# Optimization experiments

Hardware: AMD Instinct MI355X
Metric: run time of the kernel (lower is better)

The kernel has to match this reference:

```python
import jax, jax.numpy as jnp
import numpy as np

B, N, D, C, H, W = 4, 900, 256, 256, 200, 200
HEADS, LVLS, PTS, K = 8, 1, 4, 10


def setup_inputs() -> dict:
    key = jax.random.key(0)
    ks = jax.random.split(key, 16)
    s = 0.02
    return {
        "query_embed": jax.random.normal(ks[0], (B, N, D), jnp.float32),
        "ctrl_points": jax.random.uniform(ks[1], (B, N, 4, 2), jnp.float32, -50.0, 50.0),
        "bev_features": jax.random.normal(ks[2], (B, C, H, W), jnp.float32),
        "spatial_shapes": jnp.array([[H, W]], dtype=jnp.int32),
        "pc_range": jnp.array([-51.2, -51.2, -5.0, 51.2, 51.2, 3.0], jnp.float32),
        "Wq": s * jax.random.normal(ks[3], (D, D)), "bq": jnp.zeros((D,)),
        "Wv": s * jax.random.normal(ks[4], (C, D)), "bv": jnp.zeros((D,)),
        "Woff": s * jax.random.normal(ks[5], (D, HEADS * LVLS * PTS * 2)), "boff": jnp.zeros((HEADS * LVLS * PTS * 2,)),
        "Wattn": s * jax.random.normal(ks[6], (D, HEADS * LVLS * PTS)), "battn": jnp.zeros((HEADS * LVLS * PTS,)),
        "Wmo": s * jax.random.normal(ks[7], (D, D)), "bmo": jnp.zeros((D,)),
        "Wo": s * jax.random.normal(ks[8], (D, D)), "bo": jnp.zeros((D,)),
    }


def _forward(query_embed, ctrl_points, bev_features, spatial_shapes, pc_range,
             Wq, bq, Wv, bv, Woff, boff, Wattn, battn, Wmo, bmo, Wo, bo):
    b, n, d = query_embed.shape
    _, c, h, w = bev_features.shape
    hd = d // HEADS

    # --- cubic Bezier interpolation: (B,N,4,2) -> (B,N,K,2) dense points ---
    t = jnp.linspace(0.0, 1.0, K, dtype=query_embed.dtype)
    basis = jnp.stack([(1 - t) ** 3, 3 * (1 - t) ** 2 * t, 3 * (1 - t) * t ** 2, t ** 3], axis=-1)  # (K,4)
    dense = jnp.einsum('kc,bncd->bnkd', basis, ctrl_points)
    # --- normalize to [0,1] by pc_range, clamp to [0.01,0.99] ---
    nx = (dense[..., 0] - pc_range[0]) / (pc_range[3] - pc_range[0])
    ny = (dense[..., 1] - pc_range[1]) / (pc_range[4] - pc_range[1])
    ref = jnp.clip(jnp.stack([nx, ny], axis=-1), 0.01, 0.99)  # (B,N,K,2)

    # --- projections ---
    q = query_embed @ Wq + bq                                       # (B,N,D) (identity for residual)
    v = bev_features.reshape(b, c, h * w).transpose(0, 2, 1) @ Wv + bv  # (B,HW,D)
    v = v.reshape(b, h * w, HEADS, hd)

    off = (q @ Woff + boff).reshape(b, n, HEADS, LVLS, PTS, 2)
    aw = jax.nn.softmax((q @ Wattn + battn).reshape(b, n, HEADS, LVLS * PTS), axis=-1)
    aw = aw.reshape(b, n, HEADS, PTS)  # LVLS == 1

    # offset normalizer = (W, H) per level
    normalizer = jnp.stack([spatial_shapes[..., 1], spatial_shapes[..., 0]], axis=-1).astype(q.dtype)  # (L,2)
    # sampling locations: broadcast K bezier points against heads/points offsets
    loc = ref[:, :, None, :, None, :] + off / normalizer[None, None, None, :, None, :]  # (B,N,HEADS,K,PTS,2)

    # --- bilinear sampling, align_corners=False, zero padding ---
    gx = loc[..., 0] * w - 0.5
    gy = loc[..., 1] * h - 0.5
    x0 = jnp.floor(gx)
    y0 = jnp.floor(gy)
    wx = gx - x0
    wy = gy - y0
    x0i = x0.astype(jnp.int32)
    y0i = y0.astype(jnp.int32)

    vflat = v.transpose(0, 2, 1, 3).reshape(b * HEADS, h * w, hd)  # (B*HEADS, HW, hd)

    def flat(a):  # (B,N,HEADS,K,PTS) -> (B*HEADS, N*K*PTS)
        return a.transpose(0, 2, 1, 3, 4).reshape(b * HEADS, n * K * PTS)

    acc = jnp.zeros((b * HEADS, n * K * PTS, hd), dtype=q.dtype)
    for dx, dy in ((0, 0), (1, 0), (0, 1), (1, 1)):
        ix = flat(x0i) + dx
        iy = flat(y0i) + dy
        wxx = flat(wx) if dx else (1.0 - flat(wx))
        wyy = flat(wy) if dy else (1.0 - flat(wy))
        valid = (ix >= 0) & (ix < w) & (iy >= 0) & (iy < h)
        idx = jnp.clip(iy, 0, h - 1) * w + jnp.clip(ix, 0, w - 1)
        corner = jnp.take_along_axis(vflat, idx[..., None], axis=1)  # (B*HEADS, Npts, hd)
        acc = acc + corner * (wxx * wyy * valid.astype(q.dtype))[..., None]

    sampled = acc.reshape(b, HEADS, n, K, PTS, hd)
    # weighted sum over (K, PTS); attention weights shared across the K bezier points
    out = jnp.einsum('bhnkpd,bnhp->bnhd', sampled, aw).reshape(b, n, d)
    out = out @ Wmo + bmo + q   # mmcv MSDeformAttn output_proj + residual (identity = query)
    out = out @ Wo + bo         # outer output_proj
    return out


def reference(query_embed, ctrl_points, bev_features, spatial_shapes, pc_range,
              Wq, bq, Wv, bv, Woff, boff, Wattn, battn, Wmo, bmo, Wo, bo):
    return _forward(query_embed, ctrl_points, bev_features, spatial_shapes, pc_range,
                    Wq, bq, Wv, bv, Woff, boff, Wattn, battn, Wmo, bmo, Wo, bo)
```

## Files before the change

### kernel.cpp

```cpp
#include <hip/hip_runtime.h>
#include <hip/hip_bf16.h>
#include <math.h>


typedef unsigned short u16;
typedef unsigned int u32;
typedef short bf16x8 __attribute__((ext_vector_type(8)));
typedef float f32x4 __attribute__((ext_vector_type(4)));

__device__ __forceinline__ float bf2f(u16 u) {
  union { u32 i; float f; } c; c.i = ((u32)u) << 16; return c.f;
}
__device__ __forceinline__ float bflo(u32 w) {
  union { u32 i; float f; } c; c.i = w << 16; return c.f;
}
__device__ __forceinline__ float bfhi(u32 w) {
  union { u32 i; float f; } c; c.i = w & 0xffff0000u; return c.f;
}
__device__ __forceinline__ u16 f2bf(float f) {
  union { float f; u32 i; } c; c.f = f;
  u32 u = c.i;
  return (u16)((u + 0x7FFFu + ((u >> 16) & 1u)) >> 16);
}
__device__ __forceinline__ int imin(int a, int b) { return a < b ? a : b; }
__device__ __forceinline__ int imax(int a, int b) { return a > b ? a : b; }

__device__ __forceinline__ void glds16(const u16* g, u16* l) {
  __builtin_amdgcn_global_load_lds(
      (__attribute__((address_space(1))) const void*)g,
      (__attribute__((address_space(3))) void*)l, 16, 0, 0);
}

__global__ __launch_bounds__(256) void prep_weights(
    const float* __restrict__ Wq, const float* __restrict__ Wv,
    const float* __restrict__ Woff, const float* __restrict__ Wattn,
    const float* __restrict__ Wmo, const float* __restrict__ Wo,
    const float* __restrict__ boff, const float* __restrict__ battn,
    const float* __restrict__ query,
    u16* __restrict__ wqT, u16* __restrict__ wvT, u16* __restrict__ woaT,
    u16* __restrict__ wmoT, u16* __restrict__ woT, float* __restrict__ boa,
    u16* __restrict__ qin)
{
  int idx = blockIdx.x * 256 + threadIdx.x;
  {
    int i = idx * 4;
    float4 v = *(const float4*)(query + i);
    uint2 st;
    st.x = (u32)f2bf(v.x) | ((u32)f2bf(v.y) << 16);
    st.y = (u32)f2bf(v.z) | ((u32)f2bf(v.w) << 16);
    *(uint2*)(qin + i) = st;
  }
  if (idx < 65536) {
    int r = idx >> 8, c = idx & 255;
    wqT[idx]  = f2bf(Wq[c * 256 + r]);
    wvT[idx]  = f2bf(Wv[c * 256 + r]);
    wmoT[idx] = f2bf(Wmo[c * 256 + r]);
    woT[idx]  = f2bf(Wo[c * 256 + r]);
  }
  if (idx < 96 * 256) {
    int n = idx >> 8, k = idx & 255;
    woaT[idx] = f2bf((n < 64) ? Woff[k * 64 + n] : Wattn[k * 32 + (n - 64)]);
  }
  if (idx < 96) boa[idx] = (idx < 64) ? boff[idx] : battn[idx - 64];
}

__global__ __launch_bounds__(256) void transpose_bev(
    const float* __restrict__ bev, u16* __restrict__ bevT)
{
  __shared__ u16 t[64 * 66];
  const int b = blockIdx.z, c0 = blockIdx.y * 64, p0 = blockIdx.x * 64;
  const float* src = bev + ((size_t)b * 256 + c0) * 40000 + p0;
#pragma unroll
  for (int it = 0; it < 4; ++it) {
    int slot = it * 256 + threadIdx.x;
    int r = slot >> 4, i = slot & 15;
    float4 dv = *(const float4*)(src + (size_t)r * 40000 + i * 4);
    u32* dst = (u32*)&t[r * 66 + i * 4];
    dst[0] = (u32)f2bf(dv.x) | ((u32)f2bf(dv.y) << 16);
    dst[1] = (u32)f2bf(dv.z) | ((u32)f2bf(dv.w) << 16);
  }
  __syncthreads();
  u16* ob = bevT + ((size_t)b * 40000 + p0) * 256 + c0;
#pragma unroll
  for (int it = 0; it < 2; ++it) {
    int slot = it * 256 + threadIdx.x;
    int pr = slot >> 3, ci = slot & 7;
    u32 w0 = (u32)t[(ci * 8 + 0) * 66 + pr] | ((u32)t[(ci * 8 + 1) * 66 + pr] << 16);
    u32 w1 = (u32)t[(ci * 8 + 2) * 66 + pr] | ((u32)t[(ci * 8 + 3) * 66 + pr] << 16);
    u32 w2 = (u32)t[(ci * 8 + 4) * 66 + pr] | ((u32)t[(ci * 8 + 5) * 66 + pr] << 16);
    u32 w3 = (u32)t[(ci * 8 + 6) * 66 + pr] | ((u32)t[(ci * 8 + 7) * 66 + pr] << 16);
    uint4 ov; ov.x = w0; ov.y = w1; ov.z = w2; ov.w = w3;
    *(uint4*)(ob + (size_t)pr * 256 + ci * 8) = ov;
  }
}

enum { GM_F32 = 0, GM_BF16 = 1, GM_BOTH = 2, GM_V = 3 };

template <int MODE, bool HAS_RES, bool XY_SWAP>
__global__ __launch_bounds__(256) void gemm_bt(
    const u16* __restrict__ A, const u16* __restrict__ Bt,
    const float* __restrict__ bias, const float* __restrict__ res,
    u16* __restrict__ outb, float* __restrict__ outf,
    int M, int N, int K, long long btStrideZ, long long outStrideZ)
{
  __shared__ __align__(16) u16 lA[128 * 32];
  __shared__ __align__(16) u16 lB[128 * 32];
  const int tid = threadIdx.x;
  const int wv = tid >> 6, lane = tid & 63;
  const int m0 = (XY_SWAP ? blockIdx.x : blockIdx.y) * 128;
  const int n0 = (XY_SWAP ? blockIdx.y : blockIdx.x) * 128;
  const u16* Bz = Bt + (size_t)blockIdx.z * btStrideZ;

  const int crow = lane >> 2;
  const int ckoff = (lane & 3) * 8;
  const int a1 = imin(m0 + wv * 16 + crow, M - 1);
  const int a2 = imin(m0 + (wv + 4) * 16 + crow, M - 1);
  const int b1 = imin(n0 + wv * 16 + crow, N - 1);
  const int b2 = imin(n0 + (wv + 4) * 16 + crow, N - 1);
  const u16* gA1 = A + (size_t)a1 * K + ckoff;
  const u16* gA2 = A + (size_t)a2 * K + ckoff;
  const u16* gB1 = Bz + (size_t)b1 * K + ckoff;
  const u16* gB2 = Bz + (size_t)b2 * K + ckoff;
  u16* lA1 = lA + wv * 512;  u16* lA2 = lA + (wv + 4) * 512;
  u16* lB1 = lB + wv * 512;  u16* lB2 = lB + (wv + 4) * 512;

  const int fm = (wv & 1) * 64, fn = (wv >> 1) * 64;
  const int fr = lane & 15, fk = (lane >> 4) * 8;

  f32x4 acc[4][4];
#pragma unroll
  for (int i = 0; i < 4; ++i)
#pragma unroll
    for (int j = 0; j < 4; ++j) acc[i][j] = (f32x4){0.f, 0.f, 0.f, 0.f};

  for (int k0 = 0; k0 < K; k0 += 32) {
    glds16(gA1 + k0, lA1);
    glds16(gA2 + k0, lA2);
    glds16(gB1 + k0, lB1);
    glds16(gB2 + k0, lB2);
    __syncthreads();
    bf16x8 af[4], bfv[4];
#pragma unroll
    for (int i = 0; i < 4; ++i)
      af[i] = *(const bf16x8*)&lA[(fm + i * 16 + fr) * 32 + fk];
#pragma unroll
    for (int j = 0; j < 4; ++j)
      bfv[j] = *(const bf16x8*)&lB[(fn + j * 16 + fr) * 32 + fk];
    __syncthreads();
#pragma unroll
    for (int i = 0; i < 4; ++i)
#pragma unroll
      for (int j = 0; j < 4; ++j)
        acc[i][j] = __builtin_amdgcn_mfma_f32_16x16x32_bf16(af[i], bfv[j], acc[i][j], 0, 0, 0);
  }

  const int quad = lane >> 4;
#pragma unroll
  for (int j = 0; j < 4; ++j) {
    const int n = n0 + fn + j * 16 + fr;
    const bool nok = (n < N);
    float bcol = 0.f;
    if (MODE != GM_V) bcol = bias[nok ? n : 0];
#pragma unroll
    for (int i = 0; i < 4; ++i) {
      const int mb = m0 + fm + i * 16 + quad * 4;
      if (MODE == GM_V) {
        if (nok) {
          u16 u0 = f2bf(acc[i][j][0] + bias[mb + 0]);
          u16 u1 = f2bf(acc[i][j][1] + bias[mb + 1]);
          u16 u2 = f2bf(acc[i][j][2] + bias[mb + 2]);
          u16 u3 = f2bf(acc[i][j][3] + bias[mb + 3]);
          size_t off = (size_t)blockIdx.z * outStrideZ +
                       (size_t)(mb >> 5) * (40000 * 32) + (size_t)n * 32 + (mb & 31);
          uint2 st; st.x = (u32)u0 | ((u32)u1 << 16); st.y = (u32)u2 | ((u32)u3 << 16);
          *(uint2*)(outb + off) = st;
        }
      } else {
#pragma unroll
        for (int r = 0; r < 4; ++r) {
          const int m = mb + r;
          if (m < M && nok) {
            float x = acc[i][j][r] + bcol;
            if (HAS_RES) x += res[(size_t)m * N + n];
            if (MODE == GM_F32) outf[(size_t)m * N + n] = x;
            else if (MODE == GM_BF16) outb[(size_t)m * N + n] = f2bf(x);
            else { outb[(size_t)m * N + n] = f2bf(x); outf[(size_t)m * N + n] = x; }
          }
        }
      }
    }
  }
}

__global__ __launch_bounds__(256) void sampler(
    const float* __restrict__ ctrl,
    const float* __restrict__ pc,
    const float* __restrict__ oa_,
    const u16* __restrict__ v,
    u16* __restrict__ attn_out)
{
  __shared__ int   sX0[4][40], sY0[4][40];
  __shared__ float sWx[4][40], sWy[4][40], sAw[4][40];
  const int w = threadIdx.x >> 6, lane = threadIdx.x & 63;
  const int bh = blockIdx.x & 31;
  const int n = (blockIdx.x >> 5) * 4 + w;
  const int h = bh & 7, b = bh >> 3;
  const int row = b * 900 + n;

  if (lane < 40) {
    const int k = lane >> 2, p = lane & 3;
    const float t = (float)k * (1.0f / 9.0f), u = 1.f - t;
    const float c0 = u * u * u, c1 = 3.f * u * u * t, c2 = 3.f * u * t * t, c3 = t * t * t;
    const float* cp = ctrl + (size_t)row * 8;
    float cx = c0 * cp[0] + c1 * cp[2] + c2 * cp[4] + c3 * cp[6];
    float cy = c0 * cp[1] + c1 * cp[3] + c2 * cp[5] + c3 * cp[7];
    float nx = (cx - pc[0]) / (pc[3] - pc[0]);
    float ny = (cy - pc[1]) / (pc[4] - pc[1]);
    nx = fminf(fmaxf(nx, 0.01f), 0.99f);
    ny = fminf(fmaxf(ny, 0.01f), 0.99f);
    const float* oa = oa_ + (size_t)row * 96;
    float ox = oa[h * 8 + p * 2 + 0], oy = oa[h * 8 + p * 2 + 1];
    float l0 = oa[64 + h * 4 + 0], l1 = oa[64 + h * 4 + 1];
    float l2 = oa[64 + h * 4 + 2], l3 = oa[64 + h * 4 + 3];
    float mx = fmaxf(fmaxf(l0, l1), fmaxf(l2, l3));
    float e0 = __expf(l0 - mx), e1 = __expf(l1 - mx), e2 = __expf(l2 - mx), e3 = __expf(l3 - mx);
    float lp = (p == 0) ? l0 : (p == 1) ? l1 : (p == 2) ? l2 : l3;
    float aw = __expf(lp - mx) / (e0 + e1 + e2 + e3);
    float gx = (nx + ox * (1.f / 200.f)) * 200.f - 0.5f;
    float gy = (ny + oy * (1.f / 200.f)) * 200.f - 0.5f;
    float x0 = floorf(gx), y0 = floorf(gy);
    sX0[w][lane] = (int)x0; sY0[w][lane] = (int)y0;
    sWx[w][lane] = gx - x0; sWy[w][lane] = gy - y0; sAw[w][lane] = aw;
  }
  __syncthreads();

  const int sg = lane >> 3;
  const int ch0 = (lane & 7) * 4;
  const u16* vb = v + ((size_t)(b * 8 + h)) * (40000 * 32) + ch0;
  float a0 = 0.f, a1 = 0.f, a2 = 0.f, a3 = 0.f;
#pragma unroll
  for (int p = 0; p < 5; ++p) {
    const int s = p * 8 + sg;
    const int x0 = sX0[w][s], y0 = sY0[w][s];
    const float wx = sWx[w][s], wy = sWy[w][s], aw = sAw[w][s];
    const int x1 = x0 + 1, y1 = y0 + 1;
    const int cx0 = imin(imax(x0, 0), 199), cx1 = imin(imax(x1, 0), 199);
    const int cy0 = imin(imax(y0, 0), 199), cy1 = imin(imax(y1, 0), 199);
    const bool vx0 = (u32)x0 < 200u, vx1 = (u32)x1 < 200u;
    const bool vy0 = (u32)y0 < 200u, vy1 = (u32)y1 < 200u;
    const float w00 = (vx0 && vy0) ? aw * (1.f - wx) * (1.f - wy) : 0.f;
    const float w10 = (vx1 && vy0) ? aw * wx * (1.f - wy) : 0.f;
    const float w01 = (vx0 && vy1) ? aw * (1.f - wx) * wy : 0.f;
    const float w11 = (vx1 && vy1) ? aw * wx * wy : 0.f;
    uint2 d00 = *(const uint2*)(vb + (size_t)(cy0 * 200 + cx0) * 32);
    uint2 d10 = *(const uint2*)(vb + (size_t)(cy0 * 200 + cx1) * 32);
    uint2 d01 = *(const uint2*)(vb + (size_t)(cy1 * 200 + cx0) * 32);
    uint2 d11 = *(const uint2*)(vb + (size_t)(cy1 * 200 + cx1) * 32);
    a0 += w00 * bflo(d00.x) + w10 * bflo(d10.x) + w01 * bflo(d01.x) + w11 * bflo(d11.x);
    a1 += w00 * bfhi(d00.x) + w10 * bfhi(d10.x) + w01 * bfhi(d01.x) + w11 * bfhi(d11.x);
    a2 += w00 * bflo(d00.y) + w10 * bflo(d10.y) + w01 * bflo(d01.y) + w11 * bflo(d11.y);
    a3 += w00 * bfhi(d00.y) + w10 * bfhi(d10.y) + w01 * bfhi(d01.y) + w11 * bfhi(d11.y);
  }
#pragma unroll
  for (int off = 8; off < 64; off <<= 1) {
    a0 += __shfl_xor(a0, off);
    a1 += __shfl_xor(a1, off);
    a2 += __shfl_xor(a2, off);
    a3 += __shfl_xor(a3, off);
  }
  if (lane < 8) {
    uint2 st;
    st.x = (u32)f2bf(a0) | ((u32)f2bf(a1) << 16);
    st.y = (u32)f2bf(a2) | ((u32)f2bf(a3) << 16);
    *(uint2*)(attn_out + (size_t)row * 256 + h * 32 + ch0) = st;
  }
}

extern "C" void kernel_launch(void* const* d_in, const int* in_sizes, int n_in,
                              void* d_out, int out_size, void* d_ws, size_t ws_size,
                              hipStream_t stream)
{
  const float* query = (const float*)d_in[0];
  const float* ctrl  = (const float*)d_in[1];
  const float* bev   = (const float*)d_in[2];
  const float* pc    = (const float*)d_in[4];
  const float* Wq    = (const float*)d_in[5];  const float* bq    = (const float*)d_in[6];
  const float* Wv    = (const float*)d_in[7];  const float* bv    = (const float*)d_in[8];
  const float* Woff  = (const float*)d_in[9];  const float* boff  = (const float*)d_in[10];
  const float* Wattn = (const float*)d_in[11]; const float* battn = (const float*)d_in[12];
  const float* Wmo   = (const float*)d_in[13]; const float* bmo   = (const float*)d_in[14];
  const float* Wo    = (const float*)d_in[15]; const float* bo    = (const float*)d_in[16];

  char* ws = (char*)d_ws;
  size_t off = 0;
  auto alloc = [&](size_t bytes) -> void* {
    void* p = ws + off; off += (bytes + 255) & ~(size_t)255; return p;
  };
  u16*  bevT = (u16*)alloc(4ull * 40000 * 256 * 2);
  u16*  v    = (u16*)alloc(4ull * 8 * 40000 * 32 * 2);
  u16*  qin  = (u16*)alloc(3600ull * 256 * 2);
  u16*  wqT  = (u16*)alloc(65536 * 2);
  u16*  wvT  = (u16*)alloc(65536 * 2);
  u16*  woaT = (u16*)alloc(96 * 256 * 2);
  u16*  wmoT = (u16*)alloc(65536 * 2);
  u16*  woT  = (u16*)alloc(65536 * 2);
  float* boa = (float*)alloc(96 * 4);
  float* qf  = (float*)alloc(3600ull * 256 * 4);
  u16*  qb   = (u16*)alloc(3600ull * 256 * 2);
  float* oaf = (float*)alloc(3600ull * 96 * 4);
  u16*  atnO = (u16*)alloc(3600ull * 256 * 2);
  u16*  out1 = (u16*)alloc(3600ull * 256 * 2);
  (void)ws_size; (void)in_sizes; (void)n_in; (void)out_size;

  prep_weights<<<900, 256, 0, stream>>>(Wq, Wv, Woff, Wattn, Wmo, Wo, boff, battn,
                                        query, wqT, wvT, woaT, wmoT, woT, boa, qin);
  transpose_bev<<<dim3(625, 4, 4), 256, 0, stream>>>(bev, bevT);
  gemm_bt<GM_BOTH, false, false><<<dim3(2, 29, 1), 256, 0, stream>>>(
      qin, wqT, bq, nullptr, qb, qf, 3600, 256, 256, 0, 0);
  gemm_bt<GM_F32, false, false><<<dim3(1, 29, 1), 256, 0, stream>>>(
      qb, woaT, boa, nullptr, nullptr, oaf, 3600, 96, 256, 0, 0);
  gemm_bt<GM_V, false, true><<<dim3(2, 313, 4), 256, 0, stream>>>(
      wvT, bevT, bv, nullptr, v, nullptr, 256, 40000, 256,
      40000ll * 256, 8ll * 40000 * 32);
  sampler<<<7200, 256, 0, stream>>>(ctrl, pc, oaf, v, atnO);
  gemm_bt<GM_BF16, true, false><<<dim3(2, 29, 1), 256, 0, stream>>>(
      atnO, wmoT, bmo, qf, out1, nullptr, 3600, 256, 256, 0, 0);
  gemm_bt<GM_F32, false, false><<<dim3(2, 29, 1), 256, 0, stream>>>(
      out1, woT, bo, nullptr, nullptr, (float*)d_out, 3600, 256, 256, 0, 0);
}
```

Before: 416.2 us.

## Fuse BEV transpose into value GEMM and fold projection weight chains

Removes the standalone transpose_bev kernel and its bf16 intermediate. gemm_v now reads fp32 BEV directly, converts it with v_cvt_pk_bf16_f32 into swizzled LDS and prefetches the next K slice in registers. On the query side, Wq·Woff/Wattn and Wmo·Wo (plus their biases) are folded on device in prep_weights. This collapses the q, offset/attention and two output GEMMs into one 352-wide GEMM and one K=512 GEMM over a concatenated [attn | q] buffer. The trade-offs are extra per-call dot products in prep_weights and a bf16 rather than fp32 residual path.

```diff
diff --git a/kernel.cpp b/kernel.cpp
--- a/kernel.cpp
+++ b/kernel.cpp
@@ -8,9 +8,6 @@
 typedef short bf16x8 __attribute__((ext_vector_type(8)));
 typedef float f32x4 __attribute__((ext_vector_type(4)));
 
-__device__ __forceinline__ float bf2f(u16 u) {
-  union { u32 i; float f; } c; c.i = ((u32)u) << 16; return c.f;
-}
 __device__ __forceinline__ float bflo(u32 w) {
   union { u32 i; float f; } c; c.i = w << 16; return c.f;
 }
@@ -35,13 +32,14 @@
     const float* __restrict__ Wq, const float* __restrict__ Wv,
     const float* __restrict__ Woff, const float* __restrict__ Wattn,
     const float* __restrict__ Wmo, const float* __restrict__ Wo,
-    const float* __restrict__ boff, const float* __restrict__ battn,
-    const float* __restrict__ query,
-    u16* __restrict__ wqT, u16* __restrict__ wvT, u16* __restrict__ woaT,
-    u16* __restrict__ wmoT, u16* __restrict__ woT, float* __restrict__ boa,
+    const float* __restrict__ bq, const float* __restrict__ boff,
+    const float* __restrict__ battn, const float* __restrict__ bmo,
+    const float* __restrict__ bo, const float* __restrict__ query,
+    u16* __restrict__ bqoaT, u16* __restrict__ wvT, u16* __restrict__ woCat,
+    float* __restrict__ bcat, float* __restrict__ bprime,
     u16* __restrict__ qin)
 {
-  int idx = blockIdx.x * 256 + threadIdx.x;
+  const int idx = blockIdx.x * 256 + threadIdx.x;
   {
     int i = idx * 4;
     float4 v = *(const float4*)(query + i);
@@ -52,64 +50,93 @@
   }
   if (idx < 65536) {
     int r = idx >> 8, c = idx & 255;
-    wqT[idx]  = f2bf(Wq[c * 256 + r]);
-    wvT[idx]  = f2bf(Wv[c * 256 + r]);
-    wmoT[idx] = f2bf(Wmo[c * 256 + r]);
-    woT[idx]  = f2bf(Wo[c * 256 + r]);
-  }
-  if (idx < 96 * 256) {
+    bqoaT[idx] = f2bf(Wq[c * 256 + r]);
+    wvT[idx]   = f2bf(Wv[c * 256 + r]);
+  }
+  if (idx < 24576) {
     int n = idx >> 8, k = idx & 255;
-    woaT[idx] = f2bf((n < 64) ? Woff[k * 64 + n] : Wattn[k * 32 + (n - 64)]);
-  }
-  if (idx < 96) boa[idx] = (idx < 64) ? boff[idx] : battn[idx - 64];
-}
-
-__global__ __launch_bounds__(256) void transpose_bev(
-    const float* __restrict__ bev, u16* __restrict__ bevT)
-{
-  __shared__ u16 t[64 * 66];
-  const int b = blockIdx.z, c0 = blockIdx.y * 64, p0 = blockIdx.x * 64;
-  const float* src = bev + ((size_t)b * 256 + c0) * 40000 + p0;
-#pragma unroll
-  for (int it = 0; it < 4; ++it) {
-    int slot = it * 256 + threadIdx.x;
-    int r = slot >> 4, i = slot & 15;
-    float4 dv = *(const float4*)(src + (size_t)r * 40000 + i * 4);
-    u32* dst = (u32*)&t[r * 66 + i * 4];
-    dst[0] = (u32)f2bf(dv.x) | ((u32)f2bf(dv.y) << 16);
-    dst[1] = (u32)f2bf(dv.z) | ((u32)f2bf(dv.w) << 16);
-  }
-  __syncthreads();
-  u16* ob = bevT + ((size_t)b * 40000 + p0) * 256 + c0;
-#pragma unroll
-  for (int it = 0; it < 2; ++it) {
-    int slot = it * 256 + threadIdx.x;
-    int pr = slot >> 3, ci = slot & 7;
-    u32 w0 = (u32)t[(ci * 8 + 0) * 66 + pr] | ((u32)t[(ci * 8 + 1) * 66 + pr] << 16);
-    u32 w1 = (u32)t[(ci * 8 + 2) * 66 + pr] | ((u32)t[(ci * 8 + 3) * 66 + pr] << 16);
-    u32 w2 = (u32)t[(ci * 8 + 4) * 66 + pr] | ((u32)t[(ci * 8 + 5) * 66 + pr] << 16);
-    u32 w3 = (u32)t[(ci * 8 + 6) * 66 + pr] | ((u32)t[(ci * 8 + 7) * 66 + pr] << 16);
-    uint4 ov; ov.x = w0; ov.y = w1; ov.z = w2; ov.w = w3;
-    *(uint4*)(ob + (size_t)pr * 256 + ci * 8) = ov;
-  }
-}
-
-enum { GM_F32 = 0, GM_BF16 = 1, GM_BOTH = 2, GM_V = 3 };
-
-template <int MODE, bool HAS_RES, bool XY_SWAP>
+    const float* wq = Wq + k * 256;
+    float s = 0.f;
+    if (n < 64) {
+      const float* wo = Woff + n;
+#pragma unroll 4
+      for (int c = 0; c < 256; c += 4) {
+        float4 a = *(const float4*)(wq + c);
+        s += a.x * wo[(c + 0) * 64] + a.y * wo[(c + 1) * 64] +
+             a.z * wo[(c + 2) * 64] + a.w * wo[(c + 3) * 64];
+      }
+    } else {
+      const float* wa = Wattn + (n - 64);
+#pragma unroll 4
+      for (int c = 0; c < 256; c += 4) {
+        float4 a = *(const float4*)(wq + c);
+        s += a.x * wa[(c + 0) * 32] + a.y * wa[(c + 1) * 32] +
+             a.z * wa[(c + 2) * 32] + a.w * wa[(c + 3) * 32];
+      }
+    }
+    bqoaT[65536 + idx] = f2bf(s);
+  }
+  if (idx < 131072) {
+    int n = idx >> 9, k = idx & 511;
+    float s;
+    if (k >= 256) {
+      s = Wo[(size_t)(k - 256) * 256 + n];
+    } else {
+      const float* wm = Wmo + k * 256;
+      const float* wo = Wo + n;
+      s = 0.f;
+#pragma unroll 4
+      for (int c = 0; c < 256; c += 4) {
+        float4 a = *(const float4*)(wm + c);
+        s += a.x * wo[(c + 0) * 256] + a.y * wo[(c + 1) * 256] +
+             a.z * wo[(c + 2) * 256] + a.w * wo[(c + 3) * 256];
+      }
+    }
+    woCat[idx] = f2bf(s);
+  }
+  if (idx >= 131072 && idx < 131328) {
+    int n = idx - 131072;
+    const float* wo = Wo + n;
+    float s = bo[n];
+    for (int c = 0; c < 256; ++c) s += bmo[c] * wo[c * 256];
+    bprime[n] = s;
+  }
+  if (idx >= 131328 && idx < 131680) {
+    int n = idx - 131328;
+    if (n < 256) {
+      bcat[n] = bq[n];
+    } else {
+      int j = n - 256;
+      float s;
+      if (j < 64) {
+        const float* wo = Woff + j;
+        s = boff[j];
+        for (int c = 0; c < 256; ++c) s += bq[c] * wo[c * 64];
+      } else {
+        const float* wa = Wattn + (j - 64);
+        s = battn[j - 64];
+        for (int c = 0; c < 256; ++c) s += bq[c] * wa[c * 32];
+      }
+      bcat[n] = s;
+    }
+  }
+}
+
+enum { GM_F32 = 0, GM_SPLIT = 1 };
+
+template <int MODE>
 __global__ __launch_bounds__(256) void gemm_bt(
     const u16* __restrict__ A, const u16* __restrict__ Bt,
-    const float* __restrict__ bias, const float* __restrict__ res,
+    const float* __restrict__ bias,
     u16* __restrict__ outb, float* __restrict__ outf,
-    int M, int N, int K, long long btStrideZ, long long outStrideZ)
+    int M, int N, int K, int lda, int ldo)
 {
   __shared__ __align__(16) u16 lA[128 * 32];
   __shared__ __align__(16) u16 lB[128 * 32];
   const int tid = threadIdx.x;
   const int wv = tid >> 6, lane = tid & 63;
-  const int m0 = (XY_SWAP ? blockIdx.x : blockIdx.y) * 128;
-  const int n0 = (XY_SWAP ? blockIdx.y : blockIdx.x) * 128;
-  const u16* Bz = Bt + (size_t)blockIdx.z * btStrideZ;
+  const int m0 = blockIdx.y * 128;
+  const int n0 = blockIdx.x * 128;
 
   const int crow = lane >> 2;
   const int ckoff = (lane & 3) * 8;
@@ -117,10 +144,10 @@
   const int a2 = imin(m0 + (wv + 4) * 16 + crow, M - 1);
   const int b1 = imin(n0 + wv * 16 + crow, N - 1);
   const int b2 = imin(n0 + (wv + 4) * 16 + crow, N - 1);
-  const u16* gA1 = A + (size_t)a1 * K + ckoff;
-  const u16* gA2 = A + (size_t)a2 * K + ckoff;
-  const u16* gB1 = Bz + (size_t)b1 * K + ckoff;
-  const u16* gB2 = Bz + (size_t)b2 * K + ckoff;
+  const u16* gA1 = A + (size_t)a1 * lda + ckoff;
+  const u16* gA2 = A + (size_t)a2 * lda + ckoff;
+  const u16* gB1 = Bt + (size_t)b1 * K + ckoff;
+  const u16* gB2 = Bt + (size_t)b2 * K + ckoff;
   u16* lA1 = lA + wv * 512;  u16* lA2 = lA + (wv + 4) * 512;
   u16* lB1 = lB + wv * 512;  u16* lB2 = lB + (wv + 4) * 512;
 
@@ -159,34 +186,119 @@
   for (int j = 0; j < 4; ++j) {
     const int n = n0 + fn + j * 16 + fr;
     const bool nok = (n < N);
-    float bcol = 0.f;
-    if (MODE != GM_V) bcol = bias[nok ? n : 0];
+    const float bcol = bias[nok ? n : 0];
 #pragma unroll
     for (int i = 0; i < 4; ++i) {
       const int mb = m0 + fm + i * 16 + quad * 4;
-      if (MODE == GM_V) {
-        if (nok) {
-          u16 u0 = f2bf(acc[i][j][0] + bias[mb + 0]);
-          u16 u1 = f2bf(acc[i][j][1] + bias[mb + 1]);
-          u16 u2 = f2bf(acc[i][j][2] + bias[mb + 2]);
-          u16 u3 = f2bf(acc[i][j][3] + bias[mb + 3]);
-          size_t off = (size_t)blockIdx.z * outStrideZ +
-                       (size_t)(mb >> 5) * (40000 * 32) + (size_t)n * 32 + (mb & 31);
-          uint2 st; st.x = (u32)u0 | ((u32)u1 << 16); st.y = (u32)u2 | ((u32)u3 << 16);
-          *(uint2*)(outb + off) = st;
-        }
-      } else {
-#pragma unroll
-        for (int r = 0; r < 4; ++r) {
-          const int m = mb + r;
-          if (m < M && nok) {
-            float x = acc[i][j][r] + bcol;
-            if (HAS_RES) x += res[(size_t)m * N + n];
-            if (MODE == GM_F32) outf[(size_t)m * N + n] = x;
-            else if (MODE == GM_BF16) outb[(size_t)m * N + n] = f2bf(x);
-            else { outb[(size_t)m * N + n] = f2bf(x); outf[(size_t)m * N + n] = x; }
+#pragma unroll
+      for (int r = 0; r < 4; ++r) {
+        const int m = mb + r;
+        if (m < M && nok) {
+          float x = acc[i][j][r] + bcol;
+          if (MODE == GM_F32) {
+            outf[(size_t)m * ldo + n] = x;
+          } else {
+            if (n < 256) outb[(size_t)m * 512 + n] = f2bf(x);
+            else outf[(size_t)m * 96 + (n - 256)] = x;
           }
         }
+      }
+    }
+  }
+}
+
+__global__ __launch_bounds__(256) void gemm_v(
+    const u16* __restrict__ A,
+    const float* __restrict__ bev,
+    const float* __restrict__ bias,
+    u16* __restrict__ outb)
+{
+  __shared__ __align__(16) u16 lA[128 * 32];
+  __shared__ __align__(16) u16 lB[128 * 32];
+  const int tid = threadIdx.x;
+  const int wv = tid >> 6, lane = tid & 63;
+  const int m0 = blockIdx.x * 128;
+  const int n0 = blockIdx.y * 128;
+  const int z = blockIdx.z;
+
+  const int crow = lane >> 2, ckoff = (lane & 3) * 8;
+  const u16* gA1 = A + (size_t)(m0 + wv * 16 + crow) * 256 + ckoff;
+  const u16* gA2 = A + (size_t)(m0 + (wv + 4) * 16 + crow) * 256 + ckoff;
+  u16* lA1 = lA + wv * 512;  u16* lA2 = lA + (wv + 4) * 512;
+
+  const int kp = tid >> 4, nb = tid & 15;
+  const int cb = imin(n0 + nb * 8, 40000 - 8);
+  const float* src = bev + ((size_t)z * 256 + 2 * kp) * 40000 + cb;
+  const int wslot = (((kp >> 2) ^ (nb & 3)) << 2) + (kp & 3);
+  u32* lBw = (u32*)lB;
+  const int wrow = nb * 8;
+
+  const int fm = (wv & 1) * 64, fn = (wv >> 1) * 64;
+  const int fr = lane & 15, fk = (lane >> 4) * 8;
+
+  f32x4 acc[4][4];
+#pragma unroll
+  for (int i = 0; i < 4; ++i)
+#pragma unroll
+    for (int j = 0; j < 4; ++j) acc[i][j] = (f32x4){0.f, 0.f, 0.f, 0.f};
+
+  float4 r0 = *(const float4*)(src);
+  float4 r1 = *(const float4*)(src + 4);
+  float4 r2 = *(const float4*)(src + 40000);
+  float4 r3 = *(const float4*)(src + 40004);
+
+  for (int k0 = 0; k0 < 256; k0 += 32) {
+    glds16(gA1 + k0, lA1);
+    glds16(gA2 + k0, lA2);
+#define CVW(nn, a, b)                                                        \
+    { u32 pk;                                                                \
+      asm("v_cvt_pk_bf16_f32 %0, %1, %2" : "=v"(pk) : "v"(a), "v"(b));       \
+      lBw[(wrow + (nn)) * 16 + wslot] = pk; }
+    CVW(0, r0.x, r2.x) CVW(1, r0.y, r2.y) CVW(2, r0.z, r2.z) CVW(3, r0.w, r2.w)
+    CVW(4, r1.x, r3.x) CVW(5, r1.y, r3.y) CVW(6, r1.z, r3.z) CVW(7, r1.w, r3.w)
+#undef CVW
+    if (k0 < 224) {
+      const float* s2 = src + (size_t)(k0 + 32) * 40000;
+      r0 = *(const float4*)(s2);
+      r1 = *(const float4*)(s2 + 4);
+      r2 = *(const float4*)(s2 + 40000);
+      r3 = *(const float4*)(s2 + 40004);
+    }
+    __syncthreads();
+    bf16x8 af[4], bfv[4];
+#pragma unroll
+    for (int i = 0; i < 4; ++i)
+      af[i] = *(const bf16x8*)&lA[(fm + i * 16 + fr) * 32 + fk];
+#pragma unroll
+    for (int j = 0; j < 4; ++j) {
+      const int n = fn + j * 16 + fr;
+      const int pc = (((lane >> 4) ^ ((n >> 3) & 3)) << 3);
+      bfv[j] = *(const bf16x8*)&lB[n * 32 + pc];
+    }
+    __syncthreads();
+#pragma unroll
+    for (int i = 0; i < 4; ++i)
+#pragma unroll
+      for (int j = 0; j < 4; ++j)
+        acc[i][j] = __builtin_amdgcn_mfma_f32_16x16x32_bf16(af[i], bfv[j], acc[i][j], 0, 0, 0);
+  }
+
+  const int quad = lane >> 4;
+#pragma unroll
+  for (int j = 0; j < 4; ++j) {
+    const int n = n0 + fn + j * 16 + fr;
+    if (n < 40000) {
+#pragma unroll
+      for (int i = 0; i < 4; ++i) {
+        const int mb = m0 + fm + i * 16 + quad * 4;
+        u16 u0 = f2bf(acc[i][j][0] + bias[mb + 0]);
+        u16 u1 = f2bf(acc[i][j][1] + bias[mb + 1]);
+        u16 u2 = f2bf(acc[i][j][2] + bias[mb + 2]);
+        u16 u3 = f2bf(acc[i][j][3] + bias[mb + 3]);
+        size_t off = (size_t)z * (8ull * 40000 * 32) +
+                     (size_t)(mb >> 5) * (40000 * 32) + (size_t)n * 32 + (mb & 31);
+        uint2 st; st.x = (u32)u0 | ((u32)u1 << 16); st.y = (u32)u2 | ((u32)u3 << 16);
+        *(uint2*)(outb + off) = st;
       }
     }
   }
@@ -272,7 +384,7 @@
     uint2 st;
     st.x = (u32)f2bf(a0) | ((u32)f2bf(a1) << 16);
     st.y = (u32)f2bf(a2) | ((u32)f2bf(a3) << 16);
-    *(uint2*)(attn_out + (size_t)row * 256 + h * 32 + ch0) = st;
+    *(uint2*)(attn_out + (size_t)row * 512 + h * 32 + ch0) = st;
   }
 }
 
@@ -296,35 +408,24 @@
   auto alloc = [&](size_t bytes) -> void* {
     void* p = ws + off; off += (bytes + 255) & ~(size_t)255; return p;
   };
-  u16*  bevT = (u16*)alloc(4ull * 40000 * 256 * 2);
-  u16*  v    = (u16*)alloc(4ull * 8 * 40000 * 32 * 2);
-  u16*  qin  = (u16*)alloc(3600ull * 256 * 2);
-  u16*  wqT  = (u16*)alloc(65536 * 2);
-  u16*  wvT  = (u16*)alloc(65536 * 2);
-  u16*  woaT = (u16*)alloc(96 * 256 * 2);
-  u16*  wmoT = (u16*)alloc(65536 * 2);
-  u16*  woT  = (u16*)alloc(65536 * 2);
-  float* boa = (float*)alloc(96 * 4);
-  float* qf  = (float*)alloc(3600ull * 256 * 4);
-  u16*  qb   = (u16*)alloc(3600ull * 256 * 2);
-  float* oaf = (float*)alloc(3600ull * 96 * 4);
-  u16*  atnO = (u16*)alloc(3600ull * 256 * 2);
-  u16*  out1 = (u16*)alloc(3600ull * 256 * 2);
+  u16*  v     = (u16*)alloc(4ull * 8 * 40000 * 32 * 2);
+  u16*  qin   = (u16*)alloc(3600ull * 256 * 2);
+  u16*  wvT   = (u16*)alloc(65536 * 2);
+  u16*  bqoaT = (u16*)alloc(352 * 256 * 2);
+  u16*  woCat = (u16*)alloc(256 * 512 * 2);
+  float* bcat = (float*)alloc(352 * 4);
+  float* bprime = (float*)alloc(256 * 4);
+  float* oaf  = (float*)alloc(3600ull * 96 * 4);
+  u16*  qcat  = (u16*)alloc(3600ull * 512 * 2);
   (void)ws_size; (void)in_sizes; (void)n_in; (void)out_size;
 
-  prep_weights<<<900, 256, 0, stream>>>(Wq, Wv, Woff, Wattn, Wmo, Wo, boff, battn,
-                                        query, wqT, wvT, woaT, wmoT, woT, boa, qin);
-  transpose_bev<<<dim3(625, 4, 4), 256, 0, stream>>>(bev, bevT);
-  gemm_bt<GM_BOTH, false, false><<<dim3(2, 29, 1), 256, 0, stream>>>(
-      qin, wqT, bq, nullptr, qb, qf, 3600, 256, 256, 0, 0);
-  gemm_bt<GM_F32, false, false><<<dim3(1, 29, 1), 256, 0, stream>>>(
-      qb, woaT, boa, nullptr, nullptr, oaf, 3600, 96, 256, 0, 0);
-  gemm_bt<GM_V, false, true><<<dim3(2, 313, 4), 256, 0, stream>>>(
-      wvT, bevT, bv, nullptr, v, nullptr, 256, 40000, 256,
-      40000ll * 256, 8ll * 40000 * 32);
-  sampler<<<7200, 256, 0, stream>>>(ctrl, pc, oaf, v, atnO);
-  gemm_bt<GM_BF16, true, false><<<dim3(2, 29, 1), 256, 0, stream>>>(
-      atnO, wmoT, bmo, qf, out1, nullptr, 3600, 256, 256, 0, 0);
-  gemm_bt<GM_F32, false, false><<<dim3(2, 29, 1), 256, 0, stream>>>(
-      out1, woT, bo, nullptr, nullptr, (float*)d_out, 3600, 256, 256, 0, 0);
-}
+  prep_weights<<<900, 256, 0, stream>>>(Wq, Wv, Woff, Wattn, Wmo, Wo,
+                                        bq, boff, battn, bmo, bo, query,
+                                        bqoaT, wvT, woCat, bcat, bprime, qin);
+  gemm_v<<<dim3(2, 313, 4), 256, 0, stream>>>(wvT, bev, bv, v);
+  gemm_bt<GM_SPLIT><<<dim3(3, 29), 256, 0, stream>>>(
+      qin, bqoaT, bcat, qcat + 256, oaf, 3600, 352, 256, 256, 0);
+  sampler<<<7200, 256, 0, stream>>>(ctrl, pc, oaf, v, qcat);
+  gemm_bt<GM_F32><<<dim3(2, 29), 256, 0, stream>>>(
+      qcat, woCat, bprime, nullptr, (float*)d_out, 3600, 256, 512, 512, 256);
+}
```

After: 377.7 us. -9.2%, faster.
